# Kernel optimization log

Hardware: AMD Instinct MI355X
Metric: run time of the kernel (lower is better)

The kernel has to match this reference:

```python
import jax, jax.numpy as jnp
import numpy as np

B, C, T = 128, 8, 128   # batch, channels, time steps
K, S = 20, 128          # known classes, barycenter length


def setup_inputs() -> dict:
    key = jax.random.key(0)
    k1, k2, k3, k4, k5 = jax.random.split(key, 5)
    x = jax.random.normal(k1, (B, C, T), dtype=jnp.float32)
    preds = jax.random.randint(k2, (B,), 0, K).astype(jnp.int32)
    barycenters = jax.random.normal(k3, (K, S, C), dtype=jnp.float32)
    # thresholds centered near realistic scales so both detector branches fire
    top_dist = 7.0 + 0.5 * jax.random.normal(k4, (K,), dtype=jnp.float32)
    bottom_cc = 25.0 + 5.0 * jax.random.normal(k5, (K, C), dtype=jnp.float32)
    return {"x": x, "preds": preds, "barycenters": barycenters,
            "top_dist": top_dist, "bottom_cc": bottom_cc}


def _dtw_dist(cost):
    """Classic DTW DP over a [T, S] sq-euclidean cost matrix; returns accumulated cost."""
    inf = jnp.asarray(jnp.inf, cost.dtype)
    row0 = jnp.cumsum(cost[0])  # first row: only left moves

    def row_step(prev, crow):
        prev_shift = jnp.concatenate([jnp.full((1,), inf, cost.dtype), prev[:-1]])
        def col_step(left, inp):
            c, p, ps = inp
            v = c + jnp.minimum(jnp.minimum(p, ps), left)
            return v, v
        _, row = jax.lax.scan(col_step, inf, (crow, prev, prev_shift))
        return row, None

    last, _ = jax.lax.scan(row_step, row0, cost[1:])
    return last[-1]


def reference(x, preds, barycenters, top_dist, bottom_cc):
    xt = jnp.transpose(x, (0, 2, 1))                    # [B, T, C]
    x2 = jnp.sum(xt * xt, axis=-1)                      # [B, T]
    b2 = jnp.sum(barycenters * barycenters, axis=-1)    # [K, S]
    dots = jnp.einsum('btc,ksc->bkts', xt, barycenters)  # [B, K, T, S]
    cost = jnp.maximum(x2[:, None, :, None] + b2[None, :, None, :] - 2.0 * dots, 0.0)

    Bn, Kn, Tn, Sn = cost.shape
    dists = jax.vmap(_dtw_dist)(cost.reshape(Bn * Kn, Tn, Sn)).reshape(Bn, Kn)
    log_dists = jnp.log(dists)
    dtw_unknown = jnp.all(log_dists > top_dist[None, :], axis=1)   # [B]

    # per-channel full cross-correlation max vs each barycenter
    corr_max = lambda a, v: jnp.max(jnp.correlate(a, v, mode='full'))
    per_ch = jax.vmap(corr_max, in_axes=(1, 1))          # over channels -> [C]
    per_cls = jax.vmap(per_ch, in_axes=(None, 0))        # over classes  -> [K, C]
    per_b = jax.vmap(per_cls, in_axes=(0, None))         # over batch    -> [B, K, C]
    ccs = per_b(xt, barycenters)
    # class 'fails' if any channel cc is not above its bottom threshold
    cc_unknown = jnp.all(jnp.any(ccs <= bottom_cc[None, :, :], axis=2), axis=1)  # [B]

    unknown = cc_unknown | dtw_unknown
    return jnp.where(unknown, Kn, preds)
```

## Files before the change

### kernel.cpp

```cpp
#include <hip/hip_runtime.h>
#include <hip/hip_bf16.h>
#include <math.h>

#define B_ 128
#define C_ 8
#define T_ 128
#define K_ 20
#define S_ 128

#define XROW 384
#define BTROW 132
#define SWZ(j) ((j) ^ ((((j) >> 5) & 7) << 2))
#define SMEMF 2080

__global__ __launch_bounds__(64) void fused_kernel(const float* __restrict__ x,
                                                   const float* __restrict__ bary,
                                                   const float* __restrict__ top_dist,
                                                   const float* __restrict__ bottom_cc,
                                                   int* __restrict__ dtw_gt,
                                                   int* __restrict__ cc_fail2) {
    __shared__ __align__(16) float smem[SMEMF];
    const float INF = __builtin_inff();
    int u = blockIdx.x;
    int lane = threadIdx.x;

    if (u % 5 == 0) {
        int w = u / 5;
        int b = w / 10;
        int j2 = w - b * 10;
        int gl = lane & 31;
        int kk = j2 * 2 + (lane >> 5);

        #pragma unroll
        for (int i = 0; i < 4; ++i) {
            int vid = i * 64 + lane;
            int c = vid >> 5;
            int t0 = (vid & 31) << 2;
            float4 v = *(const float4*)(x + ((size_t)b * C_ + c) * T_ + t0);
            float* dst = &smem[(c >> 2) * 512 + (c & 3)];
            dst[(t0 + 0) * 4] = v.x;
            dst[(t0 + 1) * 4] = v.y;
            dst[(t0 + 2) * 4] = v.z;
            dst[(t0 + 3) * 4] = v.w;
        }
        __syncthreads();
        #pragma unroll
        for (int r = 0; r < 2; ++r) {
            int t = r * 64 + lane;
            float4 xa = *(const float4*)&smem[t * 4];
            float4 xb = *(const float4*)&smem[512 + t * 4];
            float s = xa.x * xa.x;
            s = fmaf(xa.y, xa.y, s); s = fmaf(xa.z, xa.z, s); s = fmaf(xa.w, xa.w, s);
            s = fmaf(xb.x, xb.x, s); s = fmaf(xb.y, xb.y, s); s = fmaf(xb.z, xb.z, s);
            s = fmaf(xb.w, xb.w, s);
            smem[1024 + t] = s;
        }
        __syncthreads();

        float bv[4][8], B2s[4];
        {
            const float4* bp = (const float4*)(bary + ((size_t)kk * S_ + 4 * gl) * C_);
            #pragma unroll
            for (int r = 0; r < 4; ++r) {
                float4 q0 = bp[2 * r], q1 = bp[2 * r + 1];
                bv[r][0] = q0.x; bv[r][1] = q0.y; bv[r][2] = q0.z; bv[r][3] = q0.w;
                bv[r][4] = q1.x; bv[r][5] = q1.y; bv[r][6] = q1.z; bv[r][7] = q1.w;
                float s = 0.f;
                #pragma unroll
                for (int ch = 0; ch < 8; ++ch) s = fmaf(bv[r][ch], bv[r][ch], s);
                B2s[r] = s;
                #pragma unroll
                for (int ch = 0; ch < 8; ++ch) bv[r][ch] *= -2.f;
            }
        }

        bool is0 = (gl == 0);
        float cr0 = INF, cr1 = INF, cr2 = INF, cr3 = INF;
        float lcp = is0 ? 0.f : INF;

        for (int d = 0; d < T_ + 31; ++d) {
            float lcs = __shfl_up(cr3, 1);
            float lc = is0 ? INF : lcs;
            int t = d - gl;
            if (t >= 0) {
                int tc = (t < T_ - 1) ? t : (T_ - 1);
                float bse = smem[1024 + tc];
                float4 xa = *(const float4*)&smem[tc * 4];
                float4 xb = *(const float4*)&smem[512 + tc * 4];
                float xv[8];
                xv[0] = xa.x; xv[1] = xa.y; xv[2] = xa.z; xv[3] = xa.w;
                xv[4] = xb.x; xv[5] = xb.y; xv[6] = xb.z; xv[7] = xb.w;
                float a0 = bse + B2s[0], a1 = bse + B2s[1];
                float a2 = bse + B2s[2], a3 = bse + B2s[3];
                #pragma unroll
                for (int ch = 0; ch < 8; ++ch) {
                    a0 = fmaf(bv[0][ch], xv[ch], a0);
                    a1 = fmaf(bv[1][ch], xv[ch], a1);
                    a2 = fmaf(bv[2][ch], xv[ch], a2);
                    a3 = fmaf(bv[3][ch], xv[ch], a3);
                }
                a0 = fmaxf(a0, 0.f); a1 = fmaxf(a1, 0.f);
                a2 = fmaxf(a2, 0.f); a3 = fmaxf(a3, 0.f);
                float n0 = a0 + fminf(fminf(cr0, lcp), lc);
                float n1 = a1 + fminf(fminf(cr1, cr0), n0);
                float n2 = a2 + fminf(fminf(cr2, cr1), n1);
                float n3 = a3 + fminf(fminf(cr3, cr2), n2);
                cr0 = n0; cr1 = n1; cr2 = n2; cr3 = n3;
            }
            lcp = lc;
        }

        if (gl == 31)
            dtw_gt[b * K_ + kk] = (logf(cr3) > top_dist[kk]) ? 1 : 0;
    } else {
        int idx = u - u / 5 - 1;
        int pair = idx >> 1;
        int h = idx & 1;
        int b = pair / K_;
        int kk = pair - b * K_;
        int cbase = h * 4;

        float* xp = smem;
        float* bt = smem + 4 * XROW;

        #pragma unroll
        for (int c = 0; c < 4; ++c)
            for (int j = lane; j < XROW; j += 64) {
                int t = j - (S_ - 1);
                float v = 0.f;
                if (t >= 0 && t < T_) v = x[((size_t)b * C_ + cbase + c) * T_ + t];
                xp[c * XROW + SWZ(j)] = v;
            }
        for (int i = lane; i < 4 * S_; i += 64) {
            int s = i >> 2, c = i & 3;
            bt[c * BTROW + s] = bary[((size_t)kk * S_ + s) * C_ + cbase + c];
        }
        __syncthreads();

        int cl = lane >> 4;
        int gl = lane & 15;
        int lag0 = gl << 4;
        const float* xr = xp + cl * XROW;
        const float* br = bt + cl * BTROW;

        float wdw[20];
        #pragma unroll
        for (int i = 0; i < 5; ++i) {
            float4 v = *(const float4*)&xr[SWZ(lag0 + i * 4)];
            wdw[i * 4 + 0] = v.x; wdw[i * 4 + 1] = v.y;
            wdw[i * 4 + 2] = v.z; wdw[i * 4 + 3] = v.w;
        }
        float acc[16];
        #pragma unroll
        for (int j = 0; j < 16; ++j) acc[j] = 0.f;

        #pragma unroll
        for (int s4 = 0; s4 < S_; s4 += 4) {
            float4 bq = *(const float4*)&br[s4];
            float bvals[4] = {bq.x, bq.y, bq.z, bq.w};
            #pragma unroll
            for (int uu = 0; uu < 4; ++uu) {
                #pragma unroll
                for (int j = 0; j < 16; ++j)
                    acc[j] = fmaf(wdw[uu + j], bvals[uu], acc[j]);
            }
            if (s4 < S_ - 4) {
                #pragma unroll
                for (int i = 0; i < 16; ++i) wdw[i] = wdw[i + 4];
                float4 v = *(const float4*)&xr[SWZ(lag0 + s4 + 20)];
                wdw[16] = v.x; wdw[17] = v.y; wdw[18] = v.z; wdw[19] = v.w;
            }
        }

        if (gl == 15) acc[15] = -INF;
        float m = acc[0];
        #pragma unroll
        for (int j = 1; j < 16; ++j) m = fmaxf(m, acc[j]);
        #pragma unroll
        for (int off = 8; off >= 1; off >>= 1)
            m = fmaxf(m, __shfl_xor(m, off));

        bool fail = false;
        if (gl == 0) fail = (m <= bottom_cc[kk * C_ + cbase + cl]);
        unsigned long long bal = __ballot(fail);
        if (lane == 0) cc_fail2[pair * 2 + h] = (bal != 0ULL) ? 1 : 0;
    }
}

__global__ void final_kernel(const int* __restrict__ preds,
                             const int* __restrict__ dtw_gt,
                             const int* __restrict__ cc_fail2,
                             int* __restrict__ out) {
    int b = threadIdx.x;
    if (b < B_) {
        int dtw_all = 1, cc_all = 1;
        #pragma unroll
        for (int k = 0; k < K_; ++k) {
            dtw_all &= dtw_gt[b * K_ + k];
            cc_all &= (cc_fail2[(b * K_ + k) * 2] | cc_fail2[(b * K_ + k) * 2 + 1]);
        }
        out[b] = (dtw_all | cc_all) ? K_ : preds[b];
    }
}

extern "C" void kernel_launch(void* const* d_in, const int* in_sizes, int n_in,
                              void* d_out, int out_size, void* d_ws, size_t ws_size,
                              hipStream_t stream) {
    const float* x         = (const float*)d_in[0];
    const int*   preds     = (const int*)d_in[1];
    const float* bary      = (const float*)d_in[2];
    const float* top_dist  = (const float*)d_in[3];
    const float* bottom_cc = (const float*)d_in[4];
    int* out = (int*)d_out;

    int* dtw_gt   = (int*)d_ws;
    int* cc_fail2 = dtw_gt + B_ * K_;

    fused_kernel<<<6400, 64, 0, stream>>>(x, bary, top_dist, bottom_cc, dtw_gt, cc_fail2);
    final_kernel<<<1, 128, 0, stream>>>(preds, dtw_gt, cc_fail2, out);
}
```

Baseline: 65.11 us.

## Repartition DTW wavefront to 16 lanes x 8 columns and pack 4 waves per block

Each DTW problem now uses 16 lanes holding 8 barycenter columns each, with a DPP row shift replacing the shuffle. That shortens the wavefront from 159 to 143 diagonal steps and packs four problems per wave. Blocks grow to 256 threads (4 waves), and the cross-correlation blocks share one x tile across four classes while loading the barycenter with float4 reads. The DTW inner loop now runs without the t>=0 branch by clamping indices, and the correlation loop unroll is reduced to 8. The trade-offs are more registers per thread, fewer blocks, and possible occupancy changes.

Measured after the change: 67.01 us. 1.03x slower.

```diff
diff --git a/kernel.cpp b/kernel.cpp
--- a/kernel.cpp
+++ b/kernel.cpp
@@ -8,36 +8,49 @@
 #define K_ 20
 #define S_ 128
 
-#define XROW 384
+#define XROW 388
 #define BTROW 132
 #define SWZ(j) ((j) ^ ((((j) >> 5) & 7) << 2))
-#define SMEMF 2080
-
-__global__ __launch_bounds__(64) void fused_kernel(const float* __restrict__ x,
-                                                   const float* __restrict__ bary,
-                                                   const float* __restrict__ top_dist,
-                                                   const float* __restrict__ bottom_cc,
-                                                   int* __restrict__ dtw_gt,
-                                                   int* __restrict__ cc_fail2) {
+#define XP_GUARD 16
+#define BT_BASE (4 * XROW + XP_GUARD)
+#define DTW_TILE 1152
+#define SMEMF 4608
+
+__device__ __forceinline__ float dpp_shr1(float v) {
+    int r = __builtin_amdgcn_update_dpp(0, __float_as_int(v), 0x111, 0xf, 0xf, true);
+    return __int_as_float(r);
+}
+
+__global__ __launch_bounds__(256) void fused_kernel(const float* __restrict__ x,
+                                                    const float* __restrict__ bary,
+                                                    const float* __restrict__ top_dist,
+                                                    const float* __restrict__ bottom_cc,
+                                                    int* __restrict__ dtw_gt,
+                                                    int* __restrict__ cc_fail2) {
     __shared__ __align__(16) float smem[SMEMF];
     const float INF = __builtin_inff();
     int u = blockIdx.x;
-    int lane = threadIdx.x;
-
-    if (u % 5 == 0) {
-        int w = u / 5;
-        int b = w / 10;
-        int j2 = w - b * 10;
-        int gl = lane & 31;
-        int kk = j2 * 2 + (lane >> 5);
-
-        #pragma unroll
-        for (int i = 0; i < 4; ++i) {
-            int vid = i * 64 + lane;
-            int c = vid >> 5;
-            int t0 = (vid & 31) << 2;
-            float4 v = *(const float4*)(x + ((size_t)b * C_ + c) * T_ + t0);
-            float* dst = &smem[(c >> 2) * 512 + (c & 3)];
+    int tid = threadIdx.x;
+    int w = tid >> 6;
+    int lane = tid & 63;
+
+    if (u % 9 == 0) {
+        int pg = (u / 9) * 4 + w;
+        int b  = pg / 5;
+        int kg = pg - b * 5;
+        int g  = lane >> 4;
+        int gl = lane & 15;
+        int ks = kg * 4 + g;
+        float* tile = smem + w * DTW_TILE;
+
+        const float* xb_ = x + (size_t)b * (C_ * T_);
+        #pragma unroll
+        for (int r = 0; r < 4; ++r) {
+            int f = r * 64 + lane;
+            int c = f >> 5;
+            int t0 = (f & 31) * 4;
+            float4 v = *(const float4*)(xb_ + c * T_ + t0);
+            float* dst = tile + (c >> 2) * 512 + (c & 3);
             dst[(t0 + 0) * 4] = v.x;
             dst[(t0 + 1) * 4] = v.y;
             dst[(t0 + 2) * 4] = v.z;
@@ -47,21 +60,21 @@
         #pragma unroll
         for (int r = 0; r < 2; ++r) {
             int t = r * 64 + lane;
-            float4 xa = *(const float4*)&smem[t * 4];
-            float4 xb = *(const float4*)&smem[512 + t * 4];
+            float4 xa = *(const float4*)(tile + t * 4);
+            float4 xh = *(const float4*)(tile + 512 + t * 4);
             float s = xa.x * xa.x;
             s = fmaf(xa.y, xa.y, s); s = fmaf(xa.z, xa.z, s); s = fmaf(xa.w, xa.w, s);
-            s = fmaf(xb.x, xb.x, s); s = fmaf(xb.y, xb.y, s); s = fmaf(xb.z, xb.z, s);
-            s = fmaf(xb.w, xb.w, s);
-            smem[1024 + t] = s;
+            s = fmaf(xh.x, xh.x, s); s = fmaf(xh.y, xh.y, s); s = fmaf(xh.z, xh.z, s);
+            s = fmaf(xh.w, xh.w, s);
+            tile[1024 + t] = s;
         }
         __syncthreads();
 
-        float bv[4][8], B2s[4];
+        float bv[8][8], B2s[8];
         {
-            const float4* bp = (const float4*)(bary + ((size_t)kk * S_ + 4 * gl) * C_);
-            #pragma unroll
-            for (int r = 0; r < 4; ++r) {
+            const float4* bp = (const float4*)(bary + (size_t)ks * (S_ * C_) + 64 * gl);
+            #pragma unroll
+            for (int r = 0; r < 8; ++r) {
                 float4 q0 = bp[2 * r], q1 = bp[2 * r + 1];
                 bv[r][0] = q0.x; bv[r][1] = q0.y; bv[r][2] = q0.z; bv[r][3] = q0.w;
                 bv[r][4] = q1.x; bv[r][5] = q1.y; bv[r][6] = q1.z; bv[r][7] = q1.w;
@@ -74,66 +87,74 @@
             }
         }
 
+        float cr[8];
+        #pragma unroll
+        for (int i = 0; i < 8; ++i) cr[i] = INF;
         bool is0 = (gl == 0);
-        float cr0 = INF, cr1 = INF, cr2 = INF, cr3 = INF;
         float lcp = is0 ? 0.f : INF;
 
-        for (int d = 0; d < T_ + 31; ++d) {
-            float lcs = __shfl_up(cr3, 1);
-            float lc = is0 ? INF : lcs;
+        const float* tX2 = tile + 1024;
+        for (int d = 0; d < T_ + 15; ++d) {
+            float lc = dpp_shr1(cr[7]);
+            lc = is0 ? INF : lc;
             int t = d - gl;
-            if (t >= 0) {
-                int tc = (t < T_ - 1) ? t : (T_ - 1);
-                float bse = smem[1024 + tc];
-                float4 xa = *(const float4*)&smem[tc * 4];
-                float4 xb = *(const float4*)&smem[512 + tc * 4];
-                float xv[8];
-                xv[0] = xa.x; xv[1] = xa.y; xv[2] = xa.z; xv[3] = xa.w;
-                xv[4] = xb.x; xv[5] = xb.y; xv[6] = xb.z; xv[7] = xb.w;
-                float a0 = bse + B2s[0], a1 = bse + B2s[1];
-                float a2 = bse + B2s[2], a3 = bse + B2s[3];
-                #pragma unroll
-                for (int ch = 0; ch < 8; ++ch) {
-                    a0 = fmaf(bv[0][ch], xv[ch], a0);
-                    a1 = fmaf(bv[1][ch], xv[ch], a1);
-                    a2 = fmaf(bv[2][ch], xv[ch], a2);
-                    a3 = fmaf(bv[3][ch], xv[ch], a3);
-                }
-                a0 = fmaxf(a0, 0.f); a1 = fmaxf(a1, 0.f);
-                a2 = fmaxf(a2, 0.f); a3 = fmaxf(a3, 0.f);
-                float n0 = a0 + fminf(fminf(cr0, lcp), lc);
-                float n1 = a1 + fminf(fminf(cr1, cr0), n0);
-                float n2 = a2 + fminf(fminf(cr2, cr1), n1);
-                float n3 = a3 + fminf(fminf(cr3, cr2), n2);
-                cr0 = n0; cr1 = n1; cr2 = n2; cr3 = n3;
+            int tc = t < 0 ? 0 : (t > T_ - 1 ? T_ - 1 : t);
+            float bse = tX2[tc];
+            float4 xa = *(const float4*)(tile + tc * 4);
+            float4 xh = *(const float4*)(tile + 512 + tc * 4);
+            float xv[8];
+            xv[0] = xa.x; xv[1] = xa.y; xv[2] = xa.z; xv[3] = xa.w;
+            xv[4] = xh.x; xv[5] = xh.y; xv[6] = xh.z; xv[7] = xh.w;
+            float a[8];
+            #pragma unroll
+            for (int r = 0; r < 8; ++r) {
+                float ar = bse + B2s[r];
+                #pragma unroll
+                for (int ch = 0; ch < 8; ++ch) ar = fmaf(bv[r][ch], xv[ch], ar);
+                a[r] = fmaxf(ar, 0.f);
+            }
+            float diag = lcp, left = lc;
+            #pragma unroll
+            for (int r = 0; r < 8; ++r) {
+                float n = a[r] + fminf(fminf(cr[r], diag), left);
+                diag = cr[r];
+                cr[r] = n;
+                left = n;
             }
             lcp = lc;
         }
 
-        if (gl == 31)
-            dtw_gt[b * K_ + kk] = (logf(cr3) > top_dist[kk]) ? 1 : 0;
+        if (gl == 15)
+            dtw_gt[b * K_ + ks] = (logf(cr[7]) > top_dist[ks]) ? 1 : 0;
     } else {
-        int idx = u - u / 5 - 1;
-        int pair = idx >> 1;
-        int h = idx & 1;
-        int b = pair / K_;
-        int kk = pair - b * K_;
+        int cb = u - u / 9 - 1;
+        int bh = cb / 5;
+        int g5 = cb - bh * 5;
+        int b  = bh >> 1;
+        int h  = bh & 1;
+        int kk = g5 * 4 + w;
         int cbase = h * 4;
 
         float* xp = smem;
-        float* bt = smem + 4 * XROW;
-
-        #pragma unroll
-        for (int c = 0; c < 4; ++c)
-            for (int j = lane; j < XROW; j += 64) {
+        float* bt = smem + BT_BASE + w * (4 * BTROW);
+
+        const float* xsrc = x + ((size_t)b * C_ + cbase) * T_;
+        #pragma unroll
+        for (int c = 0; c < 4; ++c) {
+            for (int j = tid; j < XROW; j += 256) {
                 int t = j - (S_ - 1);
-                float v = 0.f;
-                if (t >= 0 && t < T_) v = x[((size_t)b * C_ + cbase + c) * T_ + t];
+                float v = (t >= 0 && t < T_) ? xsrc[c * T_ + t] : 0.f;
                 xp[c * XROW + SWZ(j)] = v;
             }
-        for (int i = lane; i < 4 * S_; i += 64) {
-            int s = i >> 2, c = i & 3;
-            bt[c * BTROW + s] = bary[((size_t)kk * S_ + s) * C_ + cbase + c];
+        }
+        #pragma unroll
+        for (int r = 0; r < 2; ++r) {
+            int s = r * 64 + lane;
+            float4 q = *(const float4*)(bary + ((size_t)kk * S_ + s) * C_ + cbase);
+            bt[0 * BTROW + s] = q.x;
+            bt[1 * BTROW + s] = q.y;
+            bt[2 * BTROW + s] = q.z;
+            bt[3 * BTROW + s] = q.w;
         }
         __syncthreads();
 
@@ -154,7 +175,7 @@
         #pragma unroll
         for (int j = 0; j < 16; ++j) acc[j] = 0.f;
 
-        #pragma unroll
+        #pragma unroll 8
         for (int s4 = 0; s4 < S_; s4 += 4) {
             float4 bq = *(const float4*)&br[s4];
             float bvals[4] = {bq.x, bq.y, bq.z, bq.w};
@@ -164,12 +185,10 @@
                 for (int j = 0; j < 16; ++j)
                     acc[j] = fmaf(wdw[uu + j], bvals[uu], acc[j]);
             }
-            if (s4 < S_ - 4) {
-                #pragma unroll
-                for (int i = 0; i < 16; ++i) wdw[i] = wdw[i + 4];
-                float4 v = *(const float4*)&xr[SWZ(lag0 + s4 + 20)];
-                wdw[16] = v.x; wdw[17] = v.y; wdw[18] = v.z; wdw[19] = v.w;
-            }
+            #pragma unroll
+            for (int i = 0; i < 16; ++i) wdw[i] = wdw[i + 4];
+            float4 v = *(const float4*)&xr[SWZ(lag0 + s4 + 20)];
+            wdw[16] = v.x; wdw[17] = v.y; wdw[18] = v.z; wdw[19] = v.w;
         }
 
         if (gl == 15) acc[15] = -INF;
@@ -183,7 +202,7 @@
         bool fail = false;
         if (gl == 0) fail = (m <= bottom_cc[kk * C_ + cbase + cl]);
         unsigned long long bal = __ballot(fail);
-        if (lane == 0) cc_fail2[pair * 2 + h] = (bal != 0ULL) ? 1 : 0;
+        if (lane == 0) cc_fail2[(b * K_ + kk) * 2 + h] = (bal != 0ULL) ? 1 : 0;
     }
 }
 
@@ -216,6 +235,6 @@
     int* dtw_gt   = (int*)d_ws;
     int* cc_fail2 = dtw_gt + B_ * K_;
 
-    fused_kernel<<<6400, 64, 0, stream>>>(x, bary, top_dist, bottom_cc, dtw_gt, cc_fail2);
+    fused_kernel<<<1440, 256, 0, stream>>>(x, bary, top_dist, bottom_cc, dtw_gt, cc_fail2);
     final_kernel<<<1, 128, 0, stream>>>(preds, dtw_gt, cc_fail2, out);
 }
```
